# Optimization experiments

Measured on AMD Instinct MI355X. Metric: run time of the kernel, lower is better.

## Reference

```python
import jax, jax.numpy as jnp
import numpy as np
from jax import lax


def setup_inputs() -> dict:
    key = jax.random.key(0)
    ks = jax.random.split(key, 3)
    T, B, IC, HC, L = 512, 64, 1024, 1024, 2
    # xavier_normal-ish scale for square layers
    scale = (2.0 / (IC + HC)) ** 0.5
    x = jax.random.normal(ks[0], (T, B, IC), dtype=jnp.float32)
    Wi = jax.random.normal(ks[1], (L, HC, IC), dtype=jnp.float32) * scale
    Wh = jax.random.normal(ks[2], (L, HC, HC), dtype=jnp.float32) * scale
    bi = jnp.zeros((L, HC), dtype=jnp.float32)
    bh = jnp.zeros((L, HC), dtype=jnp.float32)
    return {"x": x, "Wi": Wi, "bi": bi, "Wh": Wh, "bh": bh}


def _run_rnn(x, Wi, bi, Wh, bh):
    # x: [T, B, ic]; Wi: [L, hc, ic]; Wh: [L, hc, hc]
    L = Wi.shape[0]
    B = x.shape[1]
    HC = Wh.shape[-1]
    seq = x
    finals = []
    for i in range(L):  # small fixed layer count
        # precompute input projection for all timesteps (one big GEMM)
        pre = jnp.einsum('tbi,hi->tbh', seq, Wi[i]) + bi[i]
        Wh_i, bh_i = Wh[i], bh[i]

        def step(h, p):
            h_new = jnp.tanh(p + h @ Wh_i.T + bh_i)
            return h_new, h_new

        h0 = jnp.zeros((B, HC), dtype=x.dtype)  # hiddens=None, learn_init=False
        h_last, seq = lax.scan(step, h0, pre)
        finals.append(h_last)
    hs = jnp.stack(finals, axis=0)  # [L, B, hc]
    return seq, hs


def reference(x, Wi, bi, Wh, bh):
    out, hs = _run_rnn(x, Wi, bi, Wh, bh)
    return out, hs
```

## Files before the change

kernel.cpp:

```cpp
#include <hip/hip_runtime.h>


#define T_STEPS 512
#define HCC     1024
#define BH      65536
#define NWG     192

typedef __attribute__((ext_vector_type(8))) short  bf16x8;
typedef __attribute__((ext_vector_type(4))) float  f32x4;

#define WF_SHORTS   8388608u
#define SLAB_SHORTS 131072u
#define OFF_H1F     WF_SHORTS
#define OFF_H2F     (OFF_H1F + 4u*SLAB_SHORTS)
#define OFF_PRE2_BYTES ((size_t)(OFF_H2F + 4u*SLAB_SHORTS) * 2u)
#define PRE2_FLOATS 65536u
#define FLG_BYTE_OFF (OFF_PRE2_BYTES + 4u*(size_t)PRE2_FLOATS*4u)
#define FLG_UINTS   (3u*64u*4u)

__device__ __forceinline__ unsigned fidx(unsigned g, unsigned i) {
    return (g * 64u + i) * 4u;
}

__device__ __forceinline__ void gload_b128_cc(bf16x8& d, const unsigned short* p) {
    asm volatile("global_load_dwordx4 %0, %1, off sc0 sc1" : "=v"(d) : "v"(p));
}
__device__ __forceinline__ void gload_f128_cc(f32x4& d, const float* p) {
    asm volatile("global_load_dwordx4 %0, %1, off sc0 sc1" : "=v"(d) : "v"(p));
}
__device__ __forceinline__ void gload_f128_nc(f32x4& d, const float* p) {
    asm volatile("global_load_dwordx4 %0, %1, off" : "=v"(d) : "v"(p));
}
__device__ __forceinline__ void gstore_b128_cc(bf16x8 v, unsigned short* p) {
    asm volatile("global_store_dwordx4 %0, %1, off sc0 sc1" :: "v"(p), "v"(v) : "memory");
}
__device__ __forceinline__ void gstore_f128_cc(f32x4 v, float* p) {
    asm volatile("global_store_dwordx4 %0, %1, off sc0 sc1" :: "v"(p), "v"(v) : "memory");
}
__device__ __forceinline__ void vm_drain()  { asm volatile("s_waitcnt vmcnt(0)"  ::: "memory"); }
__device__ __forceinline__ void vm_wait4()  { asm volatile("s_waitcnt vmcnt(4)"  ::: "memory"); }
__device__ __forceinline__ void vm_wait8()  { asm volatile("s_waitcnt vmcnt(8)"  ::: "memory"); }
__device__ __forceinline__ void vm_wait12() { asm volatile("s_waitcnt vmcnt(12)" ::: "memory"); }
#define SBAR() __builtin_amdgcn_sched_barrier(0)

__device__ __forceinline__ unsigned short bf16_rne_bits(float f) {
    unsigned u = __builtin_bit_cast(unsigned, f);
    unsigned r = u + 0x7fffu + ((u >> 16) & 1u);
    return (unsigned short)(r >> 16);
}
__device__ __forceinline__ void split1(float f, unsigned short& hi, unsigned short& lo) {
    unsigned u = __builtin_bit_cast(unsigned, f);
    unsigned r = (u + 0x7fffu + ((u >> 16) & 1u)) & 0xffff0000u;
    hi = (unsigned short)(r >> 16);
    float res = f - __builtin_bit_cast(float, r);
    lo = bf16_rne_bits(res);
}
__device__ __forceinline__ void split8(const float* f, bf16x8& H, bf16x8& L) {
#pragma unroll
    for (int e = 0; e < 8; ++e) {
        unsigned short hi, lo; split1(f[e], hi, lo);
        H[e] = (short)hi; L[e] = (short)lo;
    }
}
__device__ __forceinline__ float tanh_fast(float v) {
    float e = __expf(2.0f * v);
    return 1.0f - 2.0f * __builtin_amdgcn_rcpf(e + 1.0f);
}

__global__ __launch_bounds__(256) void zero_cnt_kernel(unsigned* cnt, unsigned n) {
    unsigned i = blockIdx.x * 256u + threadIdx.x;
    if (i < n) cnt[i] = 0u;
}

__global__ __launch_bounds__(256) void wsplit_kernel(
    const float* __restrict__ Wi, const float* __restrict__ Wh,
    unsigned short* __restrict__ WF)
{
    unsigned id  = blockIdx.x * 256u + threadIdx.x;
    unsigned kc  = id & 127u;
    unsigned row = (id >> 7) & 1023u;
    unsigned m   = id >> 17;

    const float* src = ((m & 1u) ? Wh : Wi) + (size_t)(m >> 1) * HCC * HCC
                     + (size_t)row * HCC + kc * 8u;
    float f[8];
    *(f32x4*)&f[0] = *(const f32x4*)&src[0];
    *(f32x4*)&f[4] = *(const f32x4*)&src[4];
    bf16x8 H, L; split8(f, H, L);

    unsigned c16 = row >> 4, ks = kc >> 2;
    unsigned lane = (row & 15u) + 16u * (kc & 3u);
    size_t bh_ = (((size_t)(m * 2u + 0u) * 64u + c16) * 32u + ks) * 512u + lane * 8u;
    size_t bl_ = (((size_t)(m * 2u + 1u) * 64u + c16) * 32u + ks) * 512u + lane * 8u;
    *(bf16x8*)&WF[bh_] = H;
    *(bf16x8*)&WF[bl_] = L;
}

__global__ __launch_bounds__(256) void pre1_gemm(
    const float* __restrict__ x, const float* __restrict__ bi, const float* __restrict__ bh,
    const unsigned short* __restrict__ WF, float* __restrict__ preO)
{
    __shared__ float xs[64 * 36];
    const unsigned t = blockIdx.x >> 3, cg = blockIdx.x & 7u;
    const unsigned tid = threadIdx.x, w = tid >> 6, lane = tid & 63u;
    const unsigned ct32 = cg * 4u + w;

    float b0 = bi[ct32 * 32u + (lane & 15u)]        + bh[ct32 * 32u + (lane & 15u)];
    float b1 = bi[ct32 * 32u + 16u + (lane & 15u)]  + bh[ct32 * 32u + 16u + (lane & 15u)];
    f32x4 acc[4][2];
#pragma unroll
    for (unsigned rt = 0; rt < 4; ++rt) {
        acc[rt][0] = (f32x4){b0, b0, b0, b0};
        acc[rt][1] = (f32x4){b1, b1, b1, b1};
    }
    const float* xt = x + (size_t)t * BH;

    for (unsigned ks = 0; ks < 32; ++ks) {
        {
            unsigned row = tid >> 2, c8 = (tid & 3u) * 8u;
            const float* sp = xt + (size_t)row * HCC + ks * 32u + c8;
            *(f32x4*)&xs[row * 36u + c8]      = *(const f32x4*)&sp[0];
            *(f32x4*)&xs[row * 36u + c8 + 4u] = *(const f32x4*)&sp[4];
        }
        __syncthreads();
        bf16x8 bhv[2], blv[2];
#pragma unroll
        for (unsigned c16 = 0; c16 < 2; ++c16) {
            size_t base = (((size_t)(0u) * 64u + (ct32 * 2u + c16)) * 32u + ks) * 512u + lane * 8u;
            bhv[c16] = *(const bf16x8*)&WF[base];
            blv[c16] = *(const bf16x8*)&WF[base + (size_t)64u * 32u * 512u];
        }
#pragma unroll
        for (unsigned rt = 0; rt < 4; ++rt) {
            unsigned row = rt * 16u + (lane & 15u);
            unsigned k0 = (lane >> 4) * 8u;
            float f[8];
            *(f32x4*)&f[0] = *(const f32x4*)&xs[row * 36u + k0];
            *(f32x4*)&f[4] = *(const f32x4*)&xs[row * 36u + k0 + 4u];
            bf16x8 ah, al; split8(f, ah, al);
#pragma unroll
            for (unsigned c16 = 0; c16 < 2; ++c16) {
                acc[rt][c16] = __builtin_amdgcn_mfma_f32_16x16x32_bf16(ah, bhv[c16], acc[rt][c16], 0, 0, 0);
                acc[rt][c16] = __builtin_amdgcn_mfma_f32_16x16x32_bf16(al, bhv[c16], acc[rt][c16], 0, 0, 0);
                acc[rt][c16] = __builtin_amdgcn_mfma_f32_16x16x32_bf16(ah, blv[c16], acc[rt][c16], 0, 0, 0);
            }
        }
        __syncthreads();
    }
#pragma unroll
    for (unsigned rt = 0; rt < 4; ++rt)
#pragma unroll
        for (unsigned c16 = 0; c16 < 2; ++c16) {
            unsigned rh = rt >> 1, fi = (rt & 1u) * 2u + c16;
            size_t off = ((((size_t)t * 2u + rh) * 32u + ct32) * 4u + fi) * 256u + lane * 4u;
            *(f32x4*)&preO[off] = acc[rt][c16];
        }
}

__global__ __launch_bounds__(512, 1) void rnn_persist(
    const float* __restrict__ bi, const float* __restrict__ bh,
    const unsigned short* __restrict__ WF,
    unsigned short* __restrict__ h1F, unsigned short* __restrict__ h2F,
    float* __restrict__ pre2F, unsigned* __restrict__ flg,
    float* __restrict__ seqO, float* __restrict__ hsO)
{
    __shared__ short WlS[65536];
    __shared__ float redS[7168];
    float* const epS = &redS[4096];

    const unsigned wg  = blockIdx.x;
    const unsigned grp = wg >> 6;
    const unsigned sub = wg & 63u;
    const unsigned rh  = sub >> 5, ct = sub & 31u;
    const unsigned tid = threadIdx.x;
    const unsigned w   = tid >> 6, lane = tid & 63u;

    const unsigned mat = grp + 1u;
#pragma unroll
    for (unsigned prec = 0; prec < 2; ++prec)
#pragma unroll
        for (unsigned c16l = 0; c16l < 2; ++c16l) {
            const unsigned short* sp = WF + (((size_t)(mat * 2u + prec) * 64u + (ct * 2u + c16l)) * 32u) * 512u;
            short* dp = &WlS[(prec * 2u + c16l) * 16384u];
            for (unsigned o = tid * 8u; o < 16384u; o += 4096u)
                *(bf16x8*)&dp[o] = *(const bf16x8*)&sp[o];
        }
    __syncthreads();

    float binit0 = 0.f, binit1 = 0.f;
    if (grp == 1u) {
        unsigned c = HCC + ct * 32u + (lane & 15u);
        binit0 = bi[c] + bh[c];
        binit1 = bi[c + 16u] + bh[c + 16u];
    }

    const int s0_ = (grp == 0u) ? 0 : (grp == 1u) ? 1 : 2;
    const int s1_ = s0_ + 511;

#define POLL(G, TGT) do {                                                             \
        const unsigned* fp_ = flg + fidx((G), lane);                                  \
        while (!__all((int)(__hip_atomic_load(fp_, __ATOMIC_RELAXED,                  \
                                              __HIP_MEMORY_SCOPE_AGENT) >= (unsigned)(TGT)))) \
            __builtin_amdgcn_s_sleep(1);                                              \
    } while (0)
#define POLL4(G, TGT) do {                                                            \
        const unsigned* fp_ = flg + fidx((G), rh * 32u + w * 4u + (lane & 3u));       \
        while (!__all((int)(__hip_atomic_load(fp_, __ATOMIC_RELAXED,                  \
                                              __HIP_MEMORY_SCOPE_AGENT) >= (unsigned)(TGT)))) \
            __builtin_amdgcn_s_sleep(1);                                              \
    } while (0)
#define POLL1(G, IDX, TGT) do {                                                       \
        const unsigned* fp_ = flg + fidx((G), (IDX));                                 \
        while (__hip_atomic_load(fp_, __ATOMIC_RELAXED,                               \
                                 __HIP_MEMORY_SCOPE_AGENT) < (unsigned)(TGT))         \
            __builtin_amdgcn_s_sleep(1);                                              \
    } while (0)

    for (int s = s0_; s <= s1_; ++s) {
        if (grp == 0u)      { if (s >= 1) POLL4(0u, s); }
        else if (grp == 1u) { POLL4(0u, s); }
        else {
            if (s >= 3) POLL4(2u, s);
            if (w == 0u) POLL1(1u, sub, s);
        }
        if (w == 1u) {
            if (grp == 0u && s >= 4) POLL(1u, s - 2);
            if (grp == 1u && s >= 5) POLL(2u, s - 2);
        }
        if (w == 2u) {
            if (grp == 0u && s >= 4) POLL(0u, s - 2);
            if (grp == 2u && s >= 6) POLL(2u, s - 2);
        }

        const bool do_h   = (grp == 0u) ? (s > 0) : (grp == 1u) ? true : (s > 2);
        const bool has_ld = (w == 0u && grp != 1u);

        bf16x8 Ah0[4], Ah1[4], Al0[4], Al1[4];
        if (do_h) {
            const unsigned aslot = (grp == 2u) ? ((unsigned)(s - 3) & 3u)
                                               : ((unsigned)(s - 1) & 3u);
            const unsigned short* Aslab = (grp <= 1u ? h1F : h2F)
                                        + (size_t)aslot * SLAB_SHORTS;
            const unsigned b00 = ((rh * 2u + 0u) * 2u + 0u) * 16384u;
            const unsigned b01 = ((rh * 2u + 0u) * 2u + 1u) * 16384u;
            const unsigned b10 = ((rh * 2u + 1u) * 2u + 0u) * 16384u;
            const unsigned b11 = ((rh * 2u + 1u) * 2u + 1u) * 16384u;
#pragma unroll
            for (unsigned i = 0; i < 4; ++i) {
                const unsigned ao = (w * 4u + i) * 512u + lane * 8u;
                gload_b128_cc(Ah0[i], Aslab + b00 + ao);
                gload_b128_cc(Ah1[i], Aslab + b01 + ao);
            }
#pragma unroll
            for (unsigned i = 0; i < 4; ++i) {
                const unsigned ao = (w * 4u + i) * 512u + lane * 8u;
                gload_b128_cc(Al0[i], Aslab + b10 + ao);
                gload_b128_cc(Al1[i], Aslab + b11 + ao);
            }
        }
        f32x4 ld0 = {0,0,0,0}, ld1 = {0,0,0,0}, ld2 = {0,0,0,0}, ld3 = {0,0,0,0};
        if (has_ld) {
            if (grp == 0u) {
                const float* pp = seqO + (((size_t)s * 2u + rh) * 32u + ct) * 1024u;
                gload_f128_nc(ld0, pp + 0u * 256u + lane * 4u);
                gload_f128_nc(ld1, pp + 1u * 256u + lane * 4u);
                gload_f128_nc(ld2, pp + 2u * 256u + lane * 4u);
                gload_f128_nc(ld3, pp + 3u * 256u + lane * 4u);
            } else {
                const float* pp = pre2F + (size_t)((s - 2) & 3) * PRE2_FLOATS
                                + ((size_t)rh * 32u + ct) * 1024u;
                gload_f128_cc(ld0, pp + 0u * 256u + lane * 4u);
                gload_f128_cc(ld1, pp + 1u * 256u + lane * 4u);
                gload_f128_cc(ld2, pp + 2u * 256u + lane * 4u);
                gload_f128_cc(ld3, pp + 3u * 256u + lane * 4u);
            }
        }

        f32x4 a00 = {0,0,0,0}, a01 = {0,0,0,0}, a10 = {0,0,0,0}, a11 = {0,0,0,0};
        if (do_h) {
            if (has_ld) vm_wait12(); else vm_wait8();
            SBAR();
#pragma unroll
            for (unsigned i = 0; i < 4; ++i) {
                const unsigned ao = (w * 4u + i) * 512u + lane * 8u;
                bf16x8 bh0 = *(const bf16x8*)&WlS[ao];
                bf16x8 bh1 = *(const bf16x8*)&WlS[16384u + ao];
                bf16x8 bl0 = *(const bf16x8*)&WlS[32768u + ao];
                bf16x8 bl1 = *(const bf16x8*)&WlS[49152u + ao];
                a00 = __builtin_amdgcn_mfma_f32_16x16x32_bf16(Ah0[i], bh0, a00, 0, 0, 0);
                a01 = __builtin_amdgcn_mfma_f32_16x16x32_bf16(Ah0[i], bh1, a01, 0, 0, 0);
                a10 = __builtin_amdgcn_mfma_f32_16x16x32_bf16(Ah1[i], bh0, a10, 0, 0, 0);
                a11 = __builtin_amdgcn_mfma_f32_16x16x32_bf16(Ah1[i], bh1, a11, 0, 0, 0);
                a00 = __builtin_amdgcn_mfma_f32_16x16x32_bf16(Ah0[i], bl0, a00, 0, 0, 0);
                a01 = __builtin_amdgcn_mfma_f32_16x16x32_bf16(Ah0[i], bl1, a01, 0, 0, 0);
                a10 = __builtin_amdgcn_mfma_f32_16x16x32_bf16(Ah1[i], bl0, a10, 0, 0, 0);
                a11 = __builtin_amdgcn_mfma_f32_16x16x32_bf16(Ah1[i], bl1, a11, 0, 0, 0);
            }
            if (has_ld) vm_wait4(); else vm_drain();
            SBAR();
#pragma unroll
            for (unsigned i = 0; i < 4; ++i) {
                const unsigned ao = (w * 4u + i) * 512u + lane * 8u;
                bf16x8 bh0 = *(const bf16x8*)&WlS[ao];
                bf16x8 bh1 = *(const bf16x8*)&WlS[16384u + ao];
                a00 = __builtin_amdgcn_mfma_f32_16x16x32_bf16(Al0[i], bh0, a00, 0, 0, 0);
                a01 = __builtin_amdgcn_mfma_f32_16x16x32_bf16(Al0[i], bh1, a01, 0, 0, 0);
                a10 = __builtin_amdgcn_mfma_f32_16x16x32_bf16(Al1[i], bh0, a10, 0, 0, 0);
                a11 = __builtin_amdgcn_mfma_f32_16x16x32_bf16(Al1[i], bh1, a11, 0, 0, 0);
            }
        } else {
            vm_drain(); SBAR();
        }

        if (w) {
            *(f32x4*)&redS[((w - 1u) * 4u + 0u) * 256u + lane * 4u] = a00;
            *(f32x4*)&redS[((w - 1u) * 4u + 1u) * 256u + lane * 4u] = a01;
            *(f32x4*)&redS[((w - 1u) * 4u + 2u) * 256u + lane * 4u] = a10;
            *(f32x4*)&redS[((w - 1u) * 4u + 3u) * 256u + lane * 4u] = a11;
        }
        __syncthreads();
        if (w == 0u) {
#pragma unroll
            for (unsigned b = 0; b < 7; ++b) {
                a00 += *(const f32x4*)&redS[(b * 4u + 0u) * 256u + lane * 4u];
                a01 += *(const f32x4*)&redS[(b * 4u + 1u) * 256u + lane * 4u];
                a10 += *(const f32x4*)&redS[(b * 4u + 2u) * 256u + lane * 4u];
                a11 += *(const f32x4*)&redS[(b * 4u + 3u) * 256u + lane * 4u];
            }
            vm_drain(); SBAR();
            if (grp == 1u) {
                a00 += (f32x4){binit0, binit0, binit0, binit0};
                a01 += (f32x4){binit1, binit1, binit1, binit1};
                a10 += (f32x4){binit0, binit0, binit0, binit0};
                a11 += (f32x4){binit1, binit1, binit1, binit1};
                float* pp = pre2F + (size_t)((s - 1) & 3) * PRE2_FLOATS
                          + ((size_t)rh * 32u + ct) * 1024u;
                gstore_f128_cc(a00, pp + 0u * 256u + lane * 4u);
                gstore_f128_cc(a01, pp + 1u * 256u + lane * 4u);
                gstore_f128_cc(a10, pp + 2u * 256u + lane * 4u);
                gstore_f128_cc(a11, pp + 3u * 256u + lane * 4u);
            } else {
                a00 += ld0; a01 += ld1; a10 += ld2; a11 += ld3;
#pragma unroll
                for (unsigned rr = 0; rr < 4; ++rr) {
                    unsigned rbase = ((lane >> 4) * 4u + rr) * 36u;
                    epS[rbase + (lane & 15u)]                 = tanh_fast(a00[rr]);
                    epS[rbase + 16u + (lane & 15u)]           = tanh_fast(a01[rr]);
                    epS[576u + rbase + (lane & 15u)]          = tanh_fast(a10[rr]);
                    epS[576u + rbase + 16u + (lane & 15u)]    = tanh_fast(a11[rr]);
                }
            }
        }
        if (grp != 1u) {
            __syncthreads();
            if (w < 4u) {
                const unsigned r16l = w >> 1, prec = w & 1u;
                const unsigned row = r16l * 16u + (lane & 15u);
                const unsigned c0 = (lane >> 4) * 8u;
                float f[8];
                *(f32x4*)&f[0] = *(const f32x4*)&epS[row * 36u + c0];
                *(f32x4*)&f[4] = *(const f32x4*)&epS[row * 36u + c0 + 4u];
                bf16x8 H, L; split8(f, H, L);
                unsigned short* hdst = (grp == 0u ? h1F : h2F)
                    + (size_t)((unsigned)(grp == 0u ? s : s - 2) & 3u) * SLAB_SHORTS;
                gstore_b128_cc(prec ? L : H,
                    hdst + ((rh * 2u + prec) * 2u + r16l) * 16384u + ct * 512u + lane * 8u);
            }
            if (grp == 2u) {
                const int t2 = s - 2;
#pragma unroll
                for (unsigned pass = 0; pass < 2; ++pass) {
                    const unsigned r = w * 4u + pass * 2u + (lane >> 5);
                    const unsigned c = lane & 31u;
                    const float v = epS[r * 36u + c];
                    seqO[((size_t)t2 * 64u + rh * 32u + r) * 1024u + ct * 32u + c] = v;
                    if (s == 513) hsO[BH + (size_t)(rh * 32u + r) * 1024u + ct * 32u + c] = v;
                }
            }
            if (grp == 0u && s == 511) {
#pragma unroll
                for (unsigned pass = 0; pass < 2; ++pass) {
                    const unsigned r = w * 4u + pass * 2u + (lane >> 5);
                    const unsigned c = lane & 31u;
                    hsO[(size_t)(rh * 32u + r) * 1024u + ct * 32u + c] = epS[r * 36u + c];
                }
            }
        }
        vm_drain();
        __syncthreads();
        if (tid == 0u)
            __hip_atomic_store(flg + fidx(grp, sub), (unsigned)s + 1u,
                               __ATOMIC_RELAXED, __HIP_MEMORY_SCOPE_AGENT);
    }
#undef POLL
#undef POLL4
#undef POLL1
}

extern "C" void kernel_launch(void* const* d_in, const int* in_sizes, int n_in,
                              void* d_out, int out_size, void* d_ws, size_t ws_size,
                              hipStream_t stream) {
    const float* x  = (const float*)d_in[0];
    const float* Wi = (const float*)d_in[1];
    const float* bi = (const float*)d_in[2];
    const float* Wh = (const float*)d_in[3];
    const float* bh = (const float*)d_in[4];

    float* seqO = (float*)d_out;
    float* hsO  = seqO + (size_t)T_STEPS * BH;

    unsigned short* wsS = (unsigned short*)d_ws;
    unsigned short* WF  = wsS;
    unsigned short* h1F = wsS + OFF_H1F;
    unsigned short* h2F = wsS + OFF_H2F;
    float* pre2F = (float*)((char*)d_ws + OFF_PRE2_BYTES);
    unsigned* flg = (unsigned*)((char*)d_ws + FLG_BYTE_OFF);

    zero_cnt_kernel<<<(FLG_UINTS + 255u) / 256u, 256, 0, stream>>>(flg, FLG_UINTS);
    wsplit_kernel<<<2048, 256, 0, stream>>>(Wi, Wh, WF);
    pre1_gemm<<<4096, 256, 0, stream>>>(x, bi, bh, WF, seqO);
    rnn_persist<<<NWG, 512, 0, stream>>>(bi, bh, WF, h1F, h2F, pre2F, flg, seqO, hsO);
}
```

Baseline: 2.841 ms.

## Publish per-wave readiness flags so consumers poll finer-grained producer progress

Replaces the single per-workgroup completion flag, set by thread 0 after a full drain and barrier, with per-wave flags. Each of the four store waves signals its own slice of the hidden state once its stores land. The group-1 wave signals right after its pre-activation stores, and group 2 waits only on its h stores rather than a full drain. Consumers now poll the 16 flags covering the rows they read, which shortens the critical path of the serial recurrence but multiplies flag traffic and polling work.

```diff
diff --git a/kernel.cpp b/kernel.cpp
--- a/kernel.cpp
+++ b/kernel.cpp
@@ -16,10 +16,10 @@
 #define OFF_PRE2_BYTES ((size_t)(OFF_H2F + 4u*SLAB_SHORTS) * 2u)
 #define PRE2_FLOATS 65536u
 #define FLG_BYTE_OFF (OFF_PRE2_BYTES + 4u*(size_t)PRE2_FLOATS*4u)
-#define FLG_UINTS   (3u*64u*4u)
-
-__device__ __forceinline__ unsigned fidx(unsigned g, unsigned i) {
-    return (g * 64u + i) * 4u;
+#define FLG_UINTS   (3u*64u*4u*4u)
+
+__device__ __forceinline__ unsigned fidx(unsigned g, unsigned i, unsigned wp) {
+    return ((g * 64u + i) * 4u + wp) * 4u;
 }
 
 __device__ __forceinline__ void gload_b128_cc(bf16x8& d, const unsigned short* p) {
@@ -38,6 +38,7 @@
     asm volatile("global_store_dwordx4 %0, %1, off sc0 sc1" :: "v"(p), "v"(v) : "memory");
 }
 __device__ __forceinline__ void vm_drain()  { asm volatile("s_waitcnt vmcnt(0)"  ::: "memory"); }
+__device__ __forceinline__ void vm_wait2()  { asm volatile("s_waitcnt vmcnt(2)"  ::: "memory"); }
 __device__ __forceinline__ void vm_wait4()  { asm volatile("s_waitcnt vmcnt(4)"  ::: "memory"); }
 __device__ __forceinline__ void vm_wait8()  { asm volatile("s_waitcnt vmcnt(8)"  ::: "memory"); }
 __device__ __forceinline__ void vm_wait12() { asm volatile("s_waitcnt vmcnt(12)" ::: "memory"); }
@@ -197,39 +198,40 @@
     const int s0_ = (grp == 0u) ? 0 : (grp == 1u) ? 1 : 2;
     const int s1_ = s0_ + 511;
 
-#define POLL(G, TGT) do {                                                             \
-        const unsigned* fp_ = flg + fidx((G), lane);                                  \
+#define POLL16(G, TGT) do {                                                           \
+        const unsigned* fp_ = flg + fidx((G), rh * 32u + w * 4u + ((lane >> 2) & 3u), \
+                                         lane & 3u);                                  \
         while (!__all((int)(__hip_atomic_load(fp_, __ATOMIC_RELAXED,                  \
                                               __HIP_MEMORY_SCOPE_AGENT) >= (unsigned)(TGT)))) \
             __builtin_amdgcn_s_sleep(1);                                              \
     } while (0)
-#define POLL4(G, TGT) do {                                                            \
-        const unsigned* fp_ = flg + fidx((G), rh * 32u + w * 4u + (lane & 3u));       \
+#define POLLW0(G, TGT) do {                                                           \
+        const unsigned* fp_ = flg + fidx((G), lane, 0u);                              \
         while (!__all((int)(__hip_atomic_load(fp_, __ATOMIC_RELAXED,                  \
                                               __HIP_MEMORY_SCOPE_AGENT) >= (unsigned)(TGT)))) \
             __builtin_amdgcn_s_sleep(1);                                              \
     } while (0)
 #define POLL1(G, IDX, TGT) do {                                                       \
-        const unsigned* fp_ = flg + fidx((G), (IDX));                                 \
+        const unsigned* fp_ = flg + fidx((G), (IDX), 0u);                             \
         while (__hip_atomic_load(fp_, __ATOMIC_RELAXED,                               \
                                  __HIP_MEMORY_SCOPE_AGENT) < (unsigned)(TGT))         \
             __builtin_amdgcn_s_sleep(1);                                              \
     } while (0)
 
     for (int s = s0_; s <= s1_; ++s) {
-        if (grp == 0u)      { if (s >= 1) POLL4(0u, s); }
-        else if (grp == 1u) { POLL4(0u, s); }
+        if (grp == 0u)      { if (s >= 1) POLL16(0u, s); }
+        else if (grp == 1u) { POLL16(0u, s); }
         else {
-            if (s >= 3) POLL4(2u, s);
+            if (s >= 3) POLL16(2u, s);
             if (w == 0u) POLL1(1u, sub, s);
         }
         if (w == 1u) {
-            if (grp == 0u && s >= 4) POLL(1u, s - 2);
-            if (grp == 1u && s >= 5) POLL(2u, s - 2);
+            if (grp == 0u && s >= 4) POLLW0(1u, s - 2);
+            if (grp == 1u && s >= 5) POLLW0(2u, s - 2);
         }
         if (w == 2u) {
-            if (grp == 0u && s >= 4) POLL(0u, s - 2);
-            if (grp == 2u && s >= 6) POLL(2u, s - 2);
+            if (grp == 0u && s >= 4) POLLW0(0u, s - 2);
+            if (grp == 2u && s >= 6) POLLW0(2u, s - 2);
         }
 
         const bool do_h   = (grp == 0u) ? (s > 0) : (grp == 1u) ? true : (s > 2);
@@ -339,6 +341,10 @@
                 gstore_f128_cc(a01, pp + 1u * 256u + lane * 4u);
                 gstore_f128_cc(a10, pp + 2u * 256u + lane * 4u);
                 gstore_f128_cc(a11, pp + 3u * 256u + lane * 4u);
+                vm_drain();
+                if (lane == 0u)
+                    __hip_atomic_store(flg + fidx(1u, sub, 0u), (unsigned)s + 1u,
+                                       __ATOMIC_RELAXED, __HIP_MEMORY_SCOPE_AGENT);
             } else {
                 a00 += ld0; a01 += ld1; a10 += ld2; a11 += ld3;
 #pragma unroll
@@ -385,15 +391,18 @@
                     hsO[(size_t)(rh * 32u + r) * 1024u + ct * 32u + c] = epS[r * 36u + c];
                 }
             }
-        }
-        vm_drain();
+            if (w < 4u) {
+                if (grp == 2u && s < 513) vm_wait2(); else vm_drain();
+                if (lane == 0u)
+                    __hip_atomic_store(flg + fidx(grp, sub, w), (unsigned)s + 1u,
+                                       __ATOMIC_RELAXED, __HIP_MEMORY_SCOPE_AGENT);
+            }
+        }
         __syncthreads();
-        if (tid == 0u)
-            __hip_atomic_store(flg + fidx(grp, sub), (unsigned)s + 1u,
-                               __ATOMIC_RELAXED, __HIP_MEMORY_SCOPE_AGENT);
     }
-#undef POLL
-#undef POLL4
+    vm_drain();
+#undef POLL16
+#undef POLLW0
 #undef POLL1
 }
 
```

Result: no change. 2.788 ms (-1.9%).
